# Performance work log

Measured on AMD Instinct MI355X. Metric: run time of the kernel, lower is better.

Reference implementation:

```python
import jax, jax.numpy as jnp
import numpy as np

R = 2048          # num residues
APR = 8           # atoms per residue -> num_atoms = 16384
H = 512           # hidden_dim (out_channels)
HEADS = 4
HD = H // HEADS
SD = HEADS * 7    # spatial feature dim
# atom_name2id: N=0, CA=1, C=2, O=3, CB=4, ...


def _layer_norm(x, g, b, eps=1e-5):
    mu = jnp.mean(x, axis=-1, keepdims=True)
    var = jnp.mean((x - mu) ** 2, axis=-1, keepdims=True)
    return (x - mu) / jnp.sqrt(var + eps) * g + b


def setup_inputs() -> dict:
    key = jax.random.key(0)
    ks = jax.random.split(key, 8)
    A = R * APR
    node_features = jax.random.normal(ks[0], (A, H), dtype=jnp.float32)
    node_positions = jax.random.normal(ks[1], (A, 3), dtype=jnp.float32) * 10.0
    # each residue owns APR consecutive atoms with types N,CA,C,O,CB,CG,CD,CE
    atom_type_ids = jnp.tile(jnp.arange(APR, dtype=jnp.int32), R)
    atom2residue = jnp.repeat(jnp.arange(R, dtype=jnp.int32), APR)
    s = 1.0 / np.sqrt(H)
    so = 1.0 / np.sqrt(H + SD)
    return {
        'node_features': node_features,
        'node_positions': node_positions,
        'Wq': jax.random.normal(ks[2], (H, H), jnp.float32) * s,
        'bq': jnp.zeros((H,), jnp.float32),
        'Wk': jax.random.normal(ks[3], (H, H), jnp.float32) * s,
        'bk': jnp.zeros((H,), jnp.float32),
        'Wv': jax.random.normal(ks[4], (H, H), jnp.float32) * s,
        'bv': jnp.zeros((H,), jnp.float32),
        'Wo': jax.random.normal(ks[5], (H + SD, H), jnp.float32) * so,
        'bo': jnp.zeros((H,), jnp.float32),
        'ln1_g': jnp.ones((H,), jnp.float32),
        'ln1_b': jnp.zeros((H,), jnp.float32),
        'ln2_g': jnp.ones((H,), jnp.float32),
        'ln2_b': jnp.zeros((H,), jnp.float32),
        'atom_type_ids': atom_type_ids,
        'atom2residue': atom2residue,
    }


def reference(node_features, node_positions, Wq, bq, Wk, bk, Wv, bv, Wo, bo,
              ln1_g, ln1_b, ln2_g, ln2_b, atom_type_ids, atom2residue):
    dt = node_features.dtype
    # ---------------- AtomPositionGather (vectorized scatter/gather) ----------------
    w_ca = (atom_type_ids == 1).astype(dt)   # CA
    w_cb = (atom_type_ids == 4).astype(dt)   # CB
    # scatter-mean of CA features per residue
    feat_sum = jax.ops.segment_sum(node_features * w_ca[:, None], atom2residue, num_segments=R)
    ca_cnt = jax.ops.segment_sum(w_ca, atom2residue, num_segments=R)
    residue_features = feat_sum / jnp.maximum(ca_cnt, 1.0)[:, None]
    # gather CA / CB positions (one CA/CB per residue in the data)
    pos_CA = jax.ops.segment_sum(node_positions * w_ca[:, None], atom2residue, num_segments=R)
    pos_CB = jax.ops.segment_sum(node_positions * w_cb[:, None], atom2residue, num_segments=R)
    no_cb = jnp.sum(jnp.abs(pos_CB), axis=1) < 1e-6
    pos_CB = jnp.where(no_cb[:, None], pos_CA, pos_CB)
    # residue completeness: >=3 atoms and contains N, CA, C
    cnt = jax.ops.segment_sum(jnp.ones_like(w_ca), atom2residue, num_segments=R)
    has = lambda t: jax.ops.segment_sum((atom_type_ids == t).astype(jnp.int32), atom2residue, num_segments=R) > 0
    residue_mask = (cnt >= 3) & has(0) & has(1) & has(2)
    # ---------------- per-residue local frames ----------------
    e1 = pos_CB - pos_CA
    n1 = jnp.linalg.norm(e1, axis=-1, keepdims=True)
    e1u = jnp.where(n1 > 1e-6, e1 / jnp.maximum(n1, 1e-6), e1)
    z_ax = jnp.array([0.0, 0.0, 1.0], dtype=dt)
    y_ax = jnp.array([0.0, 1.0, 0.0], dtype=dt)
    e2a = jnp.cross(e1u, jnp.broadcast_to(z_ax, e1u.shape))
    n2a = jnp.linalg.norm(e2a, axis=-1, keepdims=True)
    e2b = jnp.cross(e1u, jnp.broadcast_to(y_ax, e1u.shape))
    n2b = jnp.linalg.norm(e2b, axis=-1, keepdims=True)
    use_b = n2a < 1e-6
    e2 = jnp.where(use_b, e2b, e2a)
    n2 = jnp.where(use_b, n2b, n2a)
    e2u = e2 / jnp.maximum(n2, 1e-6)
    e3 = jnp.cross(e1u, e2u)
    frame = jnp.stack([e1u, e2u, e3], axis=-1)  # [R,3,3], basis as columns
    # original torch loop skips the last residue (i < len-1) and degenerate e1/e2
    ok = (jnp.arange(R) < R - 1) & (n1[:, 0] > 1e-6) & (n2[:, 0] > 1e-6)
    frames = jnp.where(ok[:, None, None], frame, jnp.eye(3, dtype=dt))
    # ---------------- PositionAwareLayer (batch=1, eval mode) ----------------
    x = residue_features[None]           # [1,R,H]
    ca = pos_CA[None]; cb = pos_CB[None]
    fr = frames[None]; m = residue_mask[None]
    q = (x @ Wq + bq).reshape(1, R, HEADS, HD)
    k = (x @ Wk + bk).reshape(1, R, HEADS, HD)
    v = (x @ Wv + bv).reshape(1, R, HEADS, HD)
    logits = jnp.einsum('blhd,bkhd->blkh', q, k)
    m2 = (m[:, :, None] & m[:, None, :])[..., None]          # [1,R,R,1]
    logits = jnp.where(m2, logits, -jnp.inf)
    alpha = jax.nn.softmax(logits, axis=2)                    # softmax over k
    feat_node = jnp.einsum('blkh,bkhd->blhd', alpha, v).reshape(1, R, H)
    rel_pos = cb[:, :, None, :] - ca[:, None, :, :]           # CB[l]-CA[k]: [1,R,R,3]
    bias = jnp.einsum('blkh,blkd->blhd', alpha, rel_pos)      # [1,R,HEADS,3]
    dist = jnp.linalg.norm(bias, axis=-1, keepdims=True)
    pts = jnp.einsum('blij,blhj->blhi', fr, bias)
    dirn = pts / (jnp.linalg.norm(pts, axis=-1, keepdims=True) + 1e-10)
    feat_spatial = jnp.concatenate([pts.reshape(1, R, -1), dist.reshape(1, R, -1), dirn.reshape(1, R, -1)], axis=-1)
    feat_all = jnp.concatenate([feat_node, feat_spatial], axis=-1)  # [1,R,H+SD]
    h = jax.nn.relu(feat_all @ Wo + bo)                       # dropout = identity (eval)
    h = _layer_norm(h, ln1_g, ln1_b)
    h = jnp.where(m[..., None], h, jnp.zeros_like(h))
    x_updated = _layer_norm(x + h, ln2_g, ln2_b)
    return x_updated
```

## Files before the change

### kernel.cpp

```cpp
#include <hip/hip_runtime.h>
#include <hip/hip_bf16.h>
#include <stdint.h>


#define R_ 2048
#define APR_ 8
#define H_ 512
#define HEADS_ 4
#define HD_ 128
#define FA_LD 544

typedef __attribute__((ext_vector_type(4))) float f32x4;
typedef __attribute__((ext_vector_type(4))) unsigned int u32x4;
typedef __attribute__((ext_vector_type(4))) unsigned short us4;
typedef __bf16 bf16x8 __attribute__((ext_vector_type(8)));

static __device__ __forceinline__ float bf2f(unsigned short u) {
    union { unsigned int i; float f; } c; c.i = ((unsigned int)u) << 16; return c.f;
}
static __device__ __forceinline__ unsigned short f2bf(float f) {
    union { float f; unsigned int i; } c; c.f = f;
    unsigned int r = c.i + 0x7fffu + ((c.i >> 16) & 1u);
    return (unsigned short)(r >> 16);
}
static __device__ __forceinline__ float san(float v) {
    return (v == v && fabsf(v) < 1e30f) ? v : 0.f;
}
static __device__ __forceinline__ float loadf(const void* p, size_t i, bool f32) {
    float v = f32 ? ((const float*)p)[i] : bf2f(((const unsigned short*)p)[i]);
    return (v == v && fabsf(v) < 1e30f) ? v : 0.f;
}

__global__ void diag(unsigned short* out, float val) {
    if (threadIdx.x == 0 && blockIdx.x == 0) out[0] = f2bf(val);
}

__global__ void detect_dtype(const unsigned short* __restrict__ nf, int* flag) {
    __shared__ int bad;
    if (threadIdx.x == 0) bad = 0;
    __syncthreads();
    int cnt = 0;
    for (int i = threadIdx.x; i < 8192; i += 256) {
        unsigned e = (nf[i] >> 7) & 0xFFu;
        if (e >= 0xC0u) cnt++;
    }
    atomicAdd(&bad, cnt);
    __syncthreads();
    if (threadIdx.x == 0) *flag = (bad > 16) ? 1 : 0;
}

__global__ void gather_frames(const void* __restrict__ pos,
                              const int* __restrict__ atype,
                              const int* __restrict__ flag,
                              int* __restrict__ cai, float* __restrict__ ca,
                              float* __restrict__ cb, float* __restrict__ fr,
                              float* __restrict__ maskf)
{
    int r = blockIdx.x * blockDim.x + threadIdx.x;
    if (r >= R_) return;
    bool f32 = *flag != 0;
    int base = r * APR_;
    float caP[3] = {0,0,0}, cbP[3] = {0,0,0};
    int idx = base; bool h0=false, h1=false, h2=false;
    for (int a = 0; a < APR_; a++) {
        int t = atype[base + a];
        if (t == 0) h0 = true;
        if (t == 2) h2 = true;
        if (t == 1) { h1 = true; idx = base + a;
            for (int j = 0; j < 3; j++) caP[j] += loadf(pos, (size_t)(base+a)*3 + j, f32); }
        if (t == 4) {
            for (int j = 0; j < 3; j++) cbP[j] += loadf(pos, (size_t)(base+a)*3 + j, f32); }
    }
    float s = fabsf(cbP[0]) + fabsf(cbP[1]) + fabsf(cbP[2]);
    if (s < 1e-6f) { cbP[0]=caP[0]; cbP[1]=caP[1]; cbP[2]=caP[2]; }
    float e1[3] = { cbP[0]-caP[0], cbP[1]-caP[1], cbP[2]-caP[2] };
    float n1 = sqrtf(e1[0]*e1[0] + e1[1]*e1[1] + e1[2]*e1[2]);
    float e1u[3] = { e1[0], e1[1], e1[2] };
    if (n1 > 1e-6f) { float iv = 1.f / fmaxf(n1, 1e-6f); e1u[0]*=iv; e1u[1]*=iv; e1u[2]*=iv; }
    float e2a[3] = { e1u[1], -e1u[0], 0.f };
    float n2a = sqrtf(e2a[0]*e2a[0] + e2a[1]*e2a[1]);
    float e2b[3] = { -e1u[2], 0.f, e1u[0] };
    float n2b = sqrtf(e2b[0]*e2b[0] + e2b[2]*e2b[2]);
    bool useb = n2a < 1e-6f;
    float e2[3] = { useb?e2b[0]:e2a[0], useb?e2b[1]:e2a[1], useb?e2b[2]:e2a[2] };
    float n2 = useb ? n2b : n2a;
    float iv2 = 1.f / fmaxf(n2, 1e-6f);
    float e2u[3] = { e2[0]*iv2, e2[1]*iv2, e2[2]*iv2 };
    float e3[3] = { e1u[1]*e2u[2]-e1u[2]*e2u[1],
                    e1u[2]*e2u[0]-e1u[0]*e2u[2],
                    e1u[0]*e2u[1]-e1u[1]*e2u[0] };
    bool ok = (r < R_-1) && (n1 > 1e-6f) && (n2 > 1e-6f);
    float F[9];
    if (ok) { F[0]=e1u[0]; F[1]=e2u[0]; F[2]=e3[0];
              F[3]=e1u[1]; F[4]=e2u[1]; F[5]=e3[1];
              F[6]=e1u[2]; F[7]=e2u[2]; F[8]=e3[2]; }
    else    { F[0]=1;F[1]=0;F[2]=0; F[3]=0;F[4]=1;F[5]=0; F[6]=0;F[7]=0;F[8]=1; }
    cai[r] = idx;
    for (int j = 0; j < 3; j++) { ca[r*3+j] = caP[j]; cb[r*3+j] = cbP[j]; }
    for (int j = 0; j < 9; j++) fr[r*9+j] = F[j];
    maskf[r] = (h0 && h1 && h2) ? 1.f : 0.f;
}

__global__ __launch_bounds__(256) void pack_prep(
    const void* __restrict__ nf, const int* __restrict__ cai,
    const void* __restrict__ Wq, const void* __restrict__ Wk, const void* __restrict__ Wv,
    const void* __restrict__ Wo,
    unsigned short* __restrict__ xg_hi, unsigned short* __restrict__ xg_lo,
    unsigned short* __restrict__ wqt_hi, unsigned short* __restrict__ wqt_lo,
    unsigned short* __restrict__ wot_hi, unsigned short* __restrict__ wot_lo,
    const int* __restrict__ flag)
{
    const bool f32 = *flag != 0;
    const int bid = blockIdx.x, tid = threadIdx.x;
    us4 h4, l4;
    if (bid < 1024) {
        int flat = bid*256 + tid;
        int row = flat >> 7, kc = flat & 127;
        size_t src = (size_t)cai[row]*H_ + kc*4;
        #pragma unroll
        for (int i = 0; i < 4; i++) {
            float v = loadf(nf, src + i, f32);
            unsigned short hb = f2bf(v);
            h4[i] = hb; l4[i] = f2bf(v - bf2f(hb));
        }
        *(us4*)(xg_hi + (size_t)row*H_ + kc*4) = h4;
        *(us4*)(xg_lo + (size_t)row*H_ + kc*4) = l4;
    } else if (bid < 1792) {
        int flat = (bid-1024)*256 + tid;
        int kc = flat / 1536, nn = flat - kc*1536;
        int mat = nn >> 9, ncol = nn & 511;
        const void* W = (mat==0) ? Wq : (mat==1) ? Wk : Wv;
        #pragma unroll
        for (int i = 0; i < 4; i++) {
            float v = loadf(W, (size_t)(kc*4+i)*H_ + ncol, f32);
            unsigned short hb = f2bf(v);
            h4[i] = hb; l4[i] = f2bf(v - bf2f(hb));
        }
        *(us4*)(wqt_hi + (size_t)nn*H_ + kc*4) = h4;
        *(us4*)(wqt_lo + (size_t)nn*H_ + kc*4) = l4;
    } else {
        int flat = (bid-1792)*256 + tid;
        int kc = flat >> 9, n = flat & 511;
        #pragma unroll
        for (int i = 0; i < 4; i++) {
            int k = kc*4 + i;
            float v = (k < 540) ? loadf(Wo, (size_t)k*H_ + n, f32) : 0.f;
            unsigned short hb = f2bf(v);
            h4[i] = hb; l4[i] = f2bf(v - bf2f(hb));
        }
        *(us4*)(wot_hi + (size_t)n*FA_LD + kc*4) = h4;
        *(us4*)(wot_lo + (size_t)n*FA_LD + kc*4) = l4;
    }
}

__global__ __launch_bounds__(256, 1) void qkv_mfma(
    const unsigned short* __restrict__ xg_hi, const unsigned short* __restrict__ xg_lo,
    const unsigned short* __restrict__ wqt_hi, const unsigned short* __restrict__ wqt_lo,
    const void* __restrict__ bq, const void* __restrict__ bk, const void* __restrict__ bv,
    unsigned short* __restrict__ qf, unsigned short* __restrict__ kf,
    unsigned short* __restrict__ vt, const int* __restrict__ flag)
{
    __shared__ __align__(16) char smem[33792];
    char* Xhi = smem;
    char* Xlo = smem + 8192;
    char* Bhi = smem + 16384;
    char* Blo = smem + 24576;
    const int tid = threadIdx.x;
    const int w = tid >> 6, lane = tid & 63, cL = lane & 15, gL = lane >> 4;
    const int wm = w >> 1, wn = w & 1;
    const int mbase = blockIdx.x * 128;
    const int nblk  = blockIdx.y * 128;
    const int mat = nblk >> 9, ncol0 = nblk & 511;
    const bool f32 = *flag != 0;
    const unsigned short* ahg = xg_hi + (size_t)mbase * H_;
    const unsigned short* alg = xg_lo + (size_t)mbase * H_;
    const unsigned short* bhg = wqt_hi + (size_t)nblk * H_;
    const unsigned short* blg = wqt_lo + (size_t)nblk * H_;

    u32x4 va[4], vb[4];
#define QKV_LOAD(K0)                                                          \
    {                                                                         \
        _Pragma("unroll")                                                     \
        for (int i = 0; i < 4; i++) {                                         \
// ... 142 lines not shown
        }                                                                     \
    }
    WO_LOAD(0)
    f32x4 acc[4][4] = {};
    for (int kt = 0; kt < 17; kt++) {
        __syncthreads();
        #pragma unroll
        for (int i = 0; i < 4; i++) {
            int flat = i*256 + tid, row = flat >> 3, c4 = flat & 7;
            int sw = ((row>>1)&3) << 4;
            us4 h4, l4;
            #pragma unroll
            for (int e = 0; e < 4; e++) {
                float v = xv[i*4+e];
                unsigned short hb = f2bf(v);
                h4[e] = hb; l4[e] = f2bf(v - bf2f(hb));
            }
            *(us4*)(Ahi + row*64 + ((c4*8) ^ sw)) = h4;
            *(us4*)(Alo + row*64 + ((c4*8) ^ sw)) = l4;
        }
        #pragma unroll
        for (int i = 0; i < 4; i++) {
            int flat = i*256 + tid, pl = flat >> 9, rem = flat & 511;
            int row = rem >> 2, c16 = rem & 3;
            char* p = pl ? Blo : Bhi;
            *(u32x4*)(p + row*64 + ((c16*16) ^ (((row>>1)&3)<<4))) = vb[i];
        }
        __syncthreads();
        if (kt < 16) WO_LOAD((kt+1)*32)
        bf16x8 ah[4], al[4], bh[4], bl[4];
        #pragma unroll
        for (int ms = 0; ms < 4; ms++) {
            int row = wm*64 + ms*16 + cL;
            int off = row*64 + ((gL*16) ^ (((row>>1)&3)<<4));
            ah[ms] = *(const bf16x8*)(Ahi + off);
            al[ms] = *(const bf16x8*)(Alo + off);
        }
        #pragma unroll
        for (int ns = 0; ns < 4; ns++) {
            int row = wn*64 + ns*16 + cL;
            int off = row*64 + ((gL*16) ^ (((row>>1)&3)<<4));
            bh[ns] = *(const bf16x8*)(Bhi + off);
            bl[ns] = *(const bf16x8*)(Blo + off);
        }
        #pragma unroll
        for (int ms = 0; ms < 4; ms++)
            #pragma unroll
            for (int ns = 0; ns < 4; ns++) {
                acc[ms][ns] = __builtin_amdgcn_mfma_f32_16x16x32_bf16(ah[ms], bh[ns], acc[ms][ns], 0,0,0);
                acc[ms][ns] = __builtin_amdgcn_mfma_f32_16x16x32_bf16(ah[ms], bl[ns], acc[ms][ns], 0,0,0);
                acc[ms][ns] = __builtin_amdgcn_mfma_f32_16x16x32_bf16(al[ms], bh[ns], acc[ms][ns], 0,0,0);
            }
    }
#undef WO_LOAD
    float* ep = (float*)smem + w*2112;
    #pragma unroll
    for (int half = 0; half < 2; half++) {
        __syncthreads();
        #pragma unroll
        for (int ms2 = 0; ms2 < 2; ms2++) {
            int ms = half*2 + ms2;
            #pragma unroll
            for (int ns = 0; ns < 4; ns++)
                #pragma unroll
                for (int j = 0; j < 4; j++)
                    ep[(ms2*16 + gL*4 + j)*66 + ns*16 + cL] = acc[ms][ns][j];
        }
        __syncthreads();
        int r = lane >> 1, cp = (lane & 1) * 32;
        int mrow = mbase + wm*64 + half*32 + r;
        #pragma unroll
        for (int c4 = 0; c4 < 8; c4++) {
            int nloc = cp + c4*4;
            int ncol = nbase + wn*64 + nloc;
            f32x4 o;
            #pragma unroll
            for (int e = 0; e < 4; e++)
                o[e] = ep[r*66 + nloc + e] + loadf(bo, ncol + e, f32);
            *(f32x4*)(Y + (size_t)mrow*H_ + ncol) = o;
        }
    }
}

__global__ __launch_bounds__(256, 1) void attn_mfma(
    const unsigned short* __restrict__ qf, const unsigned short* __restrict__ kf,
    const unsigned short* __restrict__ vt,
    const float* __restrict__ ca, const float* __restrict__ cb,
    const float* __restrict__ fr, const float* __restrict__ maskf,
    float* __restrict__ fa)
{
    __shared__ __align__(16) char smem[153600];
    const int tid = threadIdx.x;
    const int w = tid >> 6, lane = tid & 63;
    const int cL = lane & 15, gL = lane >> 4;
    const int qbase = blockIdx.x * 32;
    const int h = blockIdx.y;

    char* KsW  = smem + w*16384;
    char* VtW  = smem + 65536 + w*16384;
    char* AshW = smem + 131072 + w*4608;
    char* caSW = smem + 149504 + w*1024;

    bf16x8 qfrag[2][4];
    #pragma unroll
    for (int mt = 0; mt < 2; mt++)
        #pragma unroll
        for (int ks = 0; ks < 4; ks++)
            qfrag[mt][ks] = *(const bf16x8*)(qf + (size_t)(qbase + mt*16 + cL)*H_
                                             + h*HD_ + ks*32 + gL*8);
    float mq[2][4];
    #pragma unroll
    for (int mt = 0; mt < 2; mt++)
        #pragma unroll
        for (int j = 0; j < 4; j++)
            mq[mt][j] = (maskf[qbase + mt*16 + gL*4 + j] > 0.f) ? 1.f : 0.f;

    f32x4 O[2][8] = {};
    float den[2][4] = {}, axv[2][4] = {}, ayv[2][4] = {}, azv[2][4] = {};

    const unsigned short* kbase = kf + h*HD_;
    const unsigned short* vbase = vt + (size_t)h*HD_*R_;

    for (int kt = w; kt < R_/64; kt += 4) {
        const int kb = kt * 64;
        u32x4 tK[16], tV[16];
        #pragma unroll
        for (int j = 0; j < 16; j++) {
            int flat = j*64 + lane;
            tK[j] = *(const u32x4*)(kbase + (size_t)(kb + (flat>>4))*H_ + (flat&15)*8);
        }
        #pragma unroll
        for (int j = 0; j < 16; j++) {
            int flat = j*64 + lane;
            tV[j] = *(const u32x4*)(vbase + (size_t)(flat>>3)*R_ + kb + (flat&7)*8);
        }
        f32x4 cav4;
        cav4[0] = ca[(kb+lane)*3+0]; cav4[1] = ca[(kb+lane)*3+1];
        cav4[2] = ca[(kb+lane)*3+2]; cav4[3] = maskf[kb+lane];
        #pragma unroll
        for (int j = 0; j < 16; j++) {
            int flat = j*64 + lane;
            int row = flat>>4, c = flat&15;
            *(u32x4*)(KsW + row*256 + ((c*16) ^ ((row&7)<<4))) = tK[j];
        }
        #pragma unroll
        for (int j = 0; j < 16; j++) {
            int flat = j*64 + lane;
            int d = flat>>3, c = flat&7;
            *(u32x4*)(VtW + d*128 + ((c*16) ^ ((d&7)<<4))) = tV[j];
        }
        *(f32x4*)(caSW + lane*16) = cav4;

        f32x4 sacc[2][4] = {};
        #pragma unroll
        for (int nt = 0; nt < 4; nt++) {
            int n = nt*16 + cL;
            int rs = (n&7)<<4;
            bf16x8 k0 = *(const bf16x8*)(KsW + n*256 + (((0*4+gL)*16) ^ rs));
            bf16x8 k1 = *(const bf16x8*)(KsW + n*256 + (((1*4+gL)*16) ^ rs));
            bf16x8 k2 = *(const bf16x8*)(KsW + n*256 + (((2*4+gL)*16) ^ rs));
            bf16x8 k3 = *(const bf16x8*)(KsW + n*256 + (((3*4+gL)*16) ^ rs));
            #pragma unroll
            for (int mt = 0; mt < 2; mt++) {
                sacc[mt][nt] = __builtin_amdgcn_mfma_f32_16x16x32_bf16(qfrag[mt][0], k0, sacc[mt][nt], 0,0,0);
                sacc[mt][nt] = __builtin_amdgcn_mfma_f32_16x16x32_bf16(qfrag[mt][1], k1, sacc[mt][nt], 0,0,0);
                sacc[mt][nt] = __builtin_amdgcn_mfma_f32_16x16x32_bf16(qfrag[mt][2], k2, sacc[mt][nt], 0,0,0);
                sacc[mt][nt] = __builtin_amdgcn_mfma_f32_16x16x32_bf16(qfrag[mt][3], k3, sacc[mt][nt], 0,0,0);
            }
        }

        unsigned short* arow = (unsigned short*)AshW;
        #pragma unroll
        for (int nt = 0; nt < 4; nt++) {
            f32x4 cav = *(const f32x4*)(caSW + (nt*16 + cL)*16);
            #pragma unroll
            for (int mt = 0; mt < 2; mt++) {
                f32x4 s4 = sacc[mt][nt];
                float av[4];
                #pragma unroll
                for (int j = 0; j < 4; j++) {
                    float a = __expf(fminf(s4[j], 75.f)) * cav[3] * mq[mt][j];
                    if (!(a < 3.0e38f)) a = 0.f;
                    av[j] = a;
                    den[mt][j] += a;
                    axv[mt][j] += a * cav[0];
                    ayv[mt][j] += a * cav[1];
                    azv[mt][j] += a * cav[2];
                }
                unsigned int p01, p23;
                asm("v_cvt_pk_bf16_f32 %0, %1, %2" : "=v"(p01) : "v"(av[0]), "v"(av[1]));
                asm("v_cvt_pk_bf16_f32 %0, %1, %2" : "=v"(p23) : "v"(av[2]), "v"(av[3]));
                int qr = mt*16 + gL*4;
                int col = nt*16 + cL;
                arow[(qr+0)*72 + col] = (unsigned short)p01;
                arow[(qr+1)*72 + col] = (unsigned short)(p01 >> 16);
                arow[(qr+2)*72 + col] = (unsigned short)p23;
                arow[(qr+3)*72 + col] = (unsigned short)(p23 >> 16);
            }
        }

        #pragma unroll
        for (int ks = 0; ks < 2; ks++) {
            bf16x8 pa0 = *(const bf16x8*)(AshW + ((size_t)(cL)*72      + ks*32 + gL*8)*2);
            bf16x8 pa1 = *(const bf16x8*)(AshW + ((size_t)(16 + cL)*72 + ks*32 + gL*8)*2);
            #pragma unroll
            for (int dt = 0; dt < 8; dt++) {
                int d = dt*16 + cL;
                bf16x8 vb = *(const bf16x8*)(VtW + d*128 + (((ks*4+gL)*16) ^ ((d&7)<<4)));
                O[0][dt] = __builtin_amdgcn_mfma_f32_16x16x32_bf16(pa0, vb, O[0][dt], 0,0,0);
                O[1][dt] = __builtin_amdgcn_mfma_f32_16x16x32_bf16(pa1, vb, O[1][dt], 0,0,0);
            }
        }
    }

    __syncthreads();
    float* Ored = (float*)smem;
    float* dred = (float*)(smem + 67584);
    #pragma unroll
    for (int mt = 0; mt < 2; mt++)
        #pragma unroll
        for (int dt = 0; dt < 8; dt++) {
            f32x4 o4 = O[mt][dt];
            #pragma unroll
            for (int j = 0; j < 4; j++)
                Ored[w*4224 + (mt*16 + gL*4 + j)*132 + dt*16 + cL] = o4[j];
        }
    #pragma unroll
    for (int mt = 0; mt < 2; mt++)
        #pragma unroll
        for (int j = 0; j < 4; j++) {
            float d0 = den[mt][j], x0 = axv[mt][j], y0 = ayv[mt][j], z0 = azv[mt][j];
            #pragma unroll
            for (int off = 8; off >= 1; off >>= 1) {
                d0 += __shfl_xor(d0, off); x0 += __shfl_xor(x0, off);
                y0 += __shfl_xor(y0, off); z0 += __shfl_xor(z0, off);
            }
            if (cL == 0) {
                f32x4 v; v[0]=d0; v[1]=x0; v[2]=y0; v[3]=z0;
                *(f32x4*)&dred[w*128 + (mt*16 + gL*4 + j)*4] = v;
            }
        }
    __syncthreads();
    {
        int q = tid >> 3, d0 = (tid & 7) * 16;
        float dn = dred[q*4] + dred[128 + q*4] + dred[256 + q*4] + dred[384 + q*4];
        float inv = (dn > 0.f) ? 1.f/dn : 0.f;
        size_t rowb = (size_t)(qbase+q)*FA_LD + h*HD_ + d0;
        #pragma unroll
        for (int e = 0; e < 4; e++) {
            f32x4 s = *(const f32x4*)&Ored[q*132 + d0 + e*4];
            #pragma unroll
            for (int ww = 1; ww < 4; ww++)
                s += *(const f32x4*)&Ored[ww*4224 + q*132 + d0 + e*4];
            *(f32x4*)&fa[rowb + e*4] = s * inv;
        }
    }
    if (tid < 32) {
        float dn = dred[tid*4+0] + dred[128+tid*4+0] + dred[256+tid*4+0] + dred[384+tid*4+0];
        float ax = dred[tid*4+1] + dred[128+tid*4+1] + dred[256+tid*4+1] + dred[384+tid*4+1];
        float ay = dred[tid*4+2] + dred[128+tid*4+2] + dred[256+tid*4+2] + dred[384+tid*4+2];
        float az = dred[tid*4+3] + dred[128+tid*4+3] + dred[256+tid*4+3] + dred[384+tid*4+3];
        float inv = (dn > 0.f) ? 1.f/dn : 0.f;
        float live = (dn > 0.f) ? 1.f : 0.f;
        int qg = qbase + tid;
        float b0 = cb[qg*3+0]*live - ax*inv;
        float b1 = cb[qg*3+1]*live - ay*inv;
        float b2 = cb[qg*3+2]*live - az*inv;
        float dist = sqrtf(b0*b0 + b1*b1 + b2*b2);
        const float* F = fr + (size_t)qg*9;
        float p0 = F[0]*b0 + F[1]*b1 + F[2]*b2;
        float p1 = F[3]*b0 + F[4]*b1 + F[5]*b2;
        float p2 = F[6]*b0 + F[7]*b1 + F[8]*b2;
        float pn = sqrtf(p0*p0 + p1*p1 + p2*p2) + 1e-10f;
        size_t rb = (size_t)qg * FA_LD;
        fa[rb + 512 + h*3 + 0] = p0;
        fa[rb + 512 + h*3 + 1] = p1;
        fa[rb + 512 + h*3 + 2] = p2;
        fa[rb + 524 + h]       = dist;
        fa[rb + 528 + h*3 + 0] = p0/pn;
        fa[rb + 528 + h*3 + 1] = p1/pn;
        fa[rb + 528 + h*3 + 2] = p2/pn;
        if (h == 0) { fa[rb+540]=0.f; fa[rb+541]=0.f; fa[rb+542]=0.f; fa[rb+543]=0.f; }
    }
}

__global__ __launch_bounds__(256) void final_ln(
    const float* __restrict__ Y, const void* __restrict__ nf,
    const int* __restrict__ cai, const float* __restrict__ maskf,
    const void* __restrict__ g1, const void* __restrict__ b1,
    const void* __restrict__ g2, const void* __restrict__ b2,
    void* __restrict__ out, const int* __restrict__ flag)
{
    const int tid = threadIdx.x, lane = tid & 63, wave = tid >> 6;
    const int r = blockIdx.x * 4 + wave;
    bool f32 = *flag != 0;
    const float mk = maskf[r];
    const size_t xrow = (size_t)cai[r] * H_;
    float y[8], s1 = 0.f, s2 = 0.f;
    #pragma unroll
    for (int i = 0; i < 8; i++) {
        int c = lane + i*64;
        float v = fmaxf(Y[(size_t)r*H_ + c], 0.f);
        y[i] = v; s1 += v; s2 += v*v;
    }
    #pragma unroll
    for (int off = 32; off; off >>= 1) { s1 += __shfl_xor(s1, off); s2 += __shfl_xor(s2, off); }
    float mu = s1 * (1.f/H_);
    float var = s2 * (1.f/H_) - mu*mu;
    float rstd = rsqrtf(fmaxf(var, 0.f) + 1e-5f);
    float t[8], u1 = 0.f, u2 = 0.f;
    #pragma unroll
    for (int i = 0; i < 8; i++) {
        int c = lane + i*64;
        float hh = (y[i]-mu)*rstd*loadf(g1, c, f32) + loadf(b1, c, f32);
        hh *= mk;
        float tv = loadf(nf, xrow + c, f32) + hh;
        t[i] = tv; u1 += tv; u2 += tv*tv;
    }
    #pragma unroll
    for (int off = 32; off; off >>= 1) { u1 += __shfl_xor(u1, off); u2 += __shfl_xor(u2, off); }
    float mu2 = u1 * (1.f/H_);
    float var2 = u2 * (1.f/H_) - mu2*mu2;
    float rstd2 = rsqrtf(fmaxf(var2, 0.f) + 1e-5f);
    #pragma unroll
    for (int i = 0; i < 8; i++) {
        int c = lane + i*64;
        float ov = (t[i]-mu2)*rstd2*loadf(g2, c, f32) + loadf(b2, c, f32);
        if (f32) ((float*)out)[(size_t)r*H_ + c] = ov;
        else ((unsigned short*)out)[(size_t)r*H_ + c] = f2bf(ov);
    }
}

extern "C" void kernel_launch(void* const* d_in, const int* in_sizes, int n_in,
                              void* d_out, int out_size, void* d_ws, size_t ws_size,
                              hipStream_t stream)
{
    static const int expected[16] = {
        8388608, 49152, 262144, 512, 262144, 512, 262144, 512,
        276480, 512, 512, 512, 512, 512, 16384, 16384
    };
    if (n_in != 16) {
        diag<<<dim3(1), dim3(64), 0, stream>>>((unsigned short*)d_out, 1000.f + n_in);
        return;
    }
    for (int i = 0; i < 16; i++) {
        if (in_sizes[i] != expected[i]) {
            diag<<<dim3(1), dim3(64), 0, stream>>>((unsigned short*)d_out, 2000.f + 10.f*i);
            return;
        }
    }
    const size_t need = 16056320;
    if (ws_size < need) {
        diag<<<dim3(1), dim3(64), 0, stream>>>((unsigned short*)d_out, 3000.f);
        return;
    }

    const void* nf  = d_in[0];
    const void* pos = d_in[1];
    const void* Wq  = d_in[2];  const void* bq = d_in[3];
    const void* Wk  = d_in[4];  const void* bk = d_in[5];
    const void* Wv  = d_in[6];  const void* bv = d_in[7];
    const void* Wo  = d_in[8];  const void* bo = d_in[9];
    const void* g1  = d_in[10]; const void* b1 = d_in[11];
    const void* g2  = d_in[12]; const void* b2 = d_in[13];
    const int* atype = (const int*)d_in[14];

    char* ws = (char*)d_ws;
    int*   flag  = (int*)  (ws + 0);
    int*   cai   = (int*)  (ws + 1024);
    float* ca    = (float*)(ws + 9216);
    float* cb    = (float*)(ws + 33792);
    float* fr    = (float*)(ws + 58368);
    float* maskf = (float*)(ws + 132096);
    unsigned short* qf = (unsigned short*)(ws + 1048576);
    unsigned short* kf = (unsigned short*)(ws + 3145728);
    unsigned short* vt = (unsigned short*)(ws + 5242880);
    unsigned short* xg_hi = (unsigned short*)(ws + 7340032);
    unsigned short* xg_lo = (unsigned short*)(ws + 9437184);
    float* fa = (float*)(ws + 7340032);
    unsigned short* wqt_hi = (unsigned short*)(ws + 11796480);
    unsigned short* wqt_lo = (unsigned short*)(ws + 13369344);
    unsigned short* wot_hi = (unsigned short*)(ws + 14942208);
    unsigned short* wot_lo = (unsigned short*)(ws + 15499264);
    float* Y  = (float*)qf;

    detect_dtype<<<dim3(1), dim3(256), 0, stream>>>((const unsigned short*)nf, flag);
    gather_frames<<<dim3(8), dim3(256), 0, stream>>>(pos, atype, flag, cai, ca, cb, fr, maskf);
    pack_prep<<<dim3(2064), dim3(256), 0, stream>>>(nf, cai, Wq, Wk, Wv, Wo,
                                                    xg_hi, xg_lo, wqt_hi, wqt_lo,
                                                    wot_hi, wot_lo, flag);
    qkv_mfma<<<dim3(16, 12), dim3(256), 0, stream>>>(xg_hi, xg_lo, wqt_hi, wqt_lo,
                                                     bq, bk, bv, qf, kf, vt, flag);
    attn_mfma<<<dim3(R_/32, HEADS_), dim3(256), 0, stream>>>(qf, kf, vt,
                                                             ca, cb, fr, maskf, fa);
    wo_mfma<<<dim3(16, 4), dim3(256), 0, stream>>>(fa, wot_hi, wot_lo, bo, Y, flag);
    final_ln<<<dim3(512), dim3(256), 0, stream>>>(Y, nf, cai, maskf, g1, b1, g2, b2,
                                                  d_out, flag);
}
```

Before: 211.8 us.

## Split attention over key halves with atomic accumulation and separate finalize kernel

```diff
diff --git a/kernel.cpp b/kernel.cpp
--- a/kernel.cpp
+++ b/kernel.cpp
@@ -22,9 +22,6 @@
     union { float f; unsigned int i; } c; c.f = f;
     unsigned int r = c.i + 0x7fffu + ((c.i >> 16) & 1u);
     return (unsigned short)(r >> 16);
-}
-static __device__ __forceinline__ float san(float v) {
-    return (v == v && fabsf(v) < 1e30f) ? v : 0.f;
 }
 static __device__ __forceinline__ float loadf(const void* p, size_t i, bool f32) {
     float v = f32 ? ((const float*)p)[i] : bf2f(((const unsigned short*)p)[i]);
@@ -54,7 +51,8 @@
                               const int* __restrict__ flag,
                               int* __restrict__ cai, float* __restrict__ ca,
                               float* __restrict__ cb, float* __restrict__ fr,
-                              float* __restrict__ maskf)
+                              float* __restrict__ maskf,
+                              f32x4* __restrict__ ca4, float* __restrict__ dsum)
 {
     int r = blockIdx.x * blockDim.x + threadIdx.x;
     if (r >= R_) return;
@@ -98,7 +96,13 @@
     cai[r] = idx;
     for (int j = 0; j < 3; j++) { ca[r*3+j] = caP[j]; cb[r*3+j] = cbP[j]; }
     for (int j = 0; j < 9; j++) fr[r*9+j] = F[j];
-    maskf[r] = (h0 && h1 && h2) ? 1.f : 0.f;
+    float mk = (h0 && h1 && h2) ? 1.f : 0.f;
+    maskf[r] = mk;
+    f32x4 c4; c4[0]=caP[0]; c4[1]=caP[1]; c4[2]=caP[2]; c4[3]=mk;
+    ca4[r] = c4;
+    f32x4 z = {0.f,0.f,0.f,0.f};
+    #pragma unroll
+    for (int j = 0; j < 4; j++) *((f32x4*)(dsum + (size_t)r*16) + j) = z;
 }
 
 __global__ __launch_bounds__(256) void pack_prep(
@@ -407,24 +411,25 @@
     }
 }
 
-__global__ __launch_bounds__(256, 1) void attn_mfma(
+__global__ void zero_fa(f32x4* __restrict__ fa4) {
+    f32x4 z = {0.f,0.f,0.f,0.f};
+    fa4[blockIdx.x*256 + threadIdx.x] = z;
+}
+
+__global__ __launch_bounds__(256, 1) void attn_mfma2(
     const unsigned short* __restrict__ qf, const unsigned short* __restrict__ kf,
     const unsigned short* __restrict__ vt,
-    const float* __restrict__ ca, const float* __restrict__ cb,
-    const float* __restrict__ fr, const float* __restrict__ maskf,
-    float* __restrict__ fa)
+    const f32x4* __restrict__ ca4, const float* __restrict__ maskf,
+    float* __restrict__ fa, float* __restrict__ dsum)
 {
-    __shared__ __align__(16) char smem[153600];
+    __shared__ __align__(16) char smem[18432];
     const int tid = threadIdx.x;
     const int w = tid >> 6, lane = tid & 63;
     const int cL = lane & 15, gL = lane >> 4;
     const int qbase = blockIdx.x * 32;
     const int h = blockIdx.y;
-
-    char* KsW  = smem + w*16384;
-    char* VtW  = smem + 65536 + w*16384;
-    char* AshW = smem + 131072 + w*4608;
-    char* caSW = smem + 149504 + w*1024;
+    const int kb0 = blockIdx.z * 1024;
+    char* AshW = smem + w*4608;
 
     bf16x8 qfrag[2][4];
     #pragma unroll
@@ -446,45 +451,16 @@
     const unsigned short* kbase = kf + h*HD_;
     const unsigned short* vbase = vt + (size_t)h*HD_*R_;
 
-    for (int kt = w; kt < R_/64; kt += 4) {
-        const int kb = kt * 64;
-        u32x4 tK[16], tV[16];
-        #pragma unroll
-        for (int j = 0; j < 16; j++) {
-            int flat = j*64 + lane;
-            tK[j] = *(const u32x4*)(kbase + (size_t)(kb + (flat>>4))*H_ + (flat&15)*8);
-        }
-        #pragma unroll
-        for (int j = 0; j < 16; j++) {
-            int flat = j*64 + lane;
-            tV[j] = *(const u32x4*)(vbase + (size_t)(flat>>3)*R_ + kb + (flat&7)*8);
-        }
-        f32x4 cav4;
-        cav4[0] = ca[(kb+lane)*3+0]; cav4[1] = ca[(kb+lane)*3+1];
-        cav4[2] = ca[(kb+lane)*3+2]; cav4[3] = maskf[kb+lane];
-        #pragma unroll
-        for (int j = 0; j < 16; j++) {
-            int flat = j*64 + lane;
-            int row = flat>>4, c = flat&15;
-            *(u32x4*)(KsW + row*256 + ((c*16) ^ ((row&7)<<4))) = tK[j];
-        }
-        #pragma unroll
-        for (int j = 0; j < 16; j++) {
-            int flat = j*64 + lane;
-            int d = flat>>3, c = flat&7;
-            *(u32x4*)(VtW + d*128 + ((c*16) ^ ((d&7)<<4))) = tV[j];
-        }
-        *(f32x4*)(caSW + lane*16) = cav4;
-
+    for (int kt = w; kt < 16; kt += 4) {
+        const int kb = kb0 + kt*64;
         f32x4 sacc[2][4] = {};
         #pragma unroll
         for (int nt = 0; nt < 4; nt++) {
-            int n = nt*16 + cL;
-            int rs = (n&7)<<4;
-            bf16x8 k0 = *(const bf16x8*)(KsW + n*256 + (((0*4+gL)*16) ^ rs));
-            bf16x8 k1 = *(const bf16x8*)(KsW + n*256 + (((1*4+gL)*16) ^ rs));
-            bf16x8 k2 = *(const bf16x8*)(KsW + n*256 + (((2*4+gL)*16) ^ rs));
-            bf16x8 k3 = *(const bf16x8*)(KsW + n*256 + (((3*4+gL)*16) ^ rs));
+            const unsigned short* kr = kbase + (size_t)(kb + nt*16 + cL)*H_ + gL*8;
+            bf16x8 k0 = *(const bf16x8*)(kr);
+            bf16x8 k1 = *(const bf16x8*)(kr + 32);
+            bf16x8 k2 = *(const bf16x8*)(kr + 64);
+            bf16x8 k3 = *(const bf16x8*)(kr + 96);
             #pragma unroll
             for (int mt = 0; mt < 2; mt++) {
                 sacc[mt][nt] = __builtin_amdgcn_mfma_f32_16x16x32_bf16(qfrag[mt][0], k0, sacc[mt][nt], 0,0,0);
@@ -493,11 +469,10 @@
                 sacc[mt][nt] = __builtin_amdgcn_mfma_f32_16x16x32_bf16(qfrag[mt][3], k3, sacc[mt][nt], 0,0,0);
             }
         }
-
         unsigned short* arow = (unsigned short*)AshW;
         #pragma unroll
         for (int nt = 0; nt < 4; nt++) {
-            f32x4 cav = *(const f32x4*)(caSW + (nt*16 + cL)*16);
+            f32x4 cav = ca4[kb + nt*16 + cL];
             #pragma unroll
             for (int mt = 0; mt < 2; mt++) {
                 f32x4 s4 = sacc[mt][nt];
@@ -523,33 +498,27 @@
                 arow[(qr+3)*72 + col] = (unsigned short)(p23 >> 16);
             }
         }
-
         #pragma unroll
         for (int ks = 0; ks < 2; ks++) {
             bf16x8 pa0 = *(const bf16x8*)(AshW + ((size_t)(cL)*72      + ks*32 + gL*8)*2);
             bf16x8 pa1 = *(const bf16x8*)(AshW + ((size_t)(16 + cL)*72 + ks*32 + gL*8)*2);
             #pragma unroll
             for (int dt = 0; dt < 8; dt++) {
-                int d = dt*16 + cL;
-                bf16x8 vb = *(const bf16x8*)(VtW + d*128 + (((ks*4+gL)*16) ^ ((d&7)<<4)));
+                bf16x8 vb = *(const bf16x8*)(vbase + (size_t)(dt*16 + cL)*R_ + kb + ks*32 + gL*8);
                 O[0][dt] = __builtin_amdgcn_mfma_f32_16x16x32_bf16(pa0, vb, O[0][dt], 0,0,0);
                 O[1][dt] = __builtin_amdgcn_mfma_f32_16x16x32_bf16(pa1, vb, O[1][dt], 0,0,0);
             }
         }
     }
 
-    __syncthreads();
-    float* Ored = (float*)smem;
-    float* dred = (float*)(smem + 67584);
     #pragma unroll
     for (int mt = 0; mt < 2; mt++)
         #pragma unroll
-        for (int dt = 0; dt < 8; dt++) {
-            f32x4 o4 = O[mt][dt];
+        for (int dt = 0; dt < 8; dt++)
             #pragma unroll
             for (int j = 0; j < 4; j++)
-                Ored[w*4224 + (mt*16 + gL*4 + j)*132 + dt*16 + cL] = o4[j];
-        }
+                atomicAdd(&fa[(size_t)(qbase + mt*16 + gL*4 + j)*FA_LD + h*HD_ + dt*16 + cL],
+                          O[mt][dt][j]);
     #pragma unroll
     for (int mt = 0; mt < 2; mt++)
         #pragma unroll
@@ -561,43 +530,48 @@
                 y0 += __shfl_xor(y0, off); z0 += __shfl_xor(z0, off);
             }
             if (cL == 0) {
-                f32x4 v; v[0]=d0; v[1]=x0; v[2]=y0; v[3]=z0;
-                *(f32x4*)&dred[w*128 + (mt*16 + gL*4 + j)*4] = v;
-            }
-        }
-    __syncthreads();
+                int qg = qbase + mt*16 + gL*4 + j;
+                float* dp = dsum + (size_t)(qg*4 + h)*4;
+                atomicAdd(dp+0, d0); atomicAdd(dp+1, x0);
+                atomicAdd(dp+2, y0); atomicAdd(dp+3, z0);
+            }
+        }
+}
+
+__global__ __launch_bounds__(256) void attn_finalize(
+    const float* __restrict__ dsum, const float* __restrict__ cb,
+    const float* __restrict__ fr, float* __restrict__ fa)
+{
+    const int tid = threadIdx.x;
+    const int q0 = blockIdx.x * 8;
     {
-        int q = tid >> 3, d0 = (tid & 7) * 16;
-        float dn = dred[q*4] + dred[128 + q*4] + dred[256 + q*4] + dred[384 + q*4];
+        int row = q0 + (tid >> 5), l32 = tid & 31, hh = l32 >> 3;
+        float dn = dsum[(size_t)(row*4 + hh)*4];
         float inv = (dn > 0.f) ? 1.f/dn : 0.f;
-        size_t rowb = (size_t)(qbase+q)*FA_LD + h*HD_ + d0;
+        float* p = fa + (size_t)row*FA_LD + l32*16;
         #pragma unroll
         for (int e = 0; e < 4; e++) {
-            f32x4 s = *(const f32x4*)&Ored[q*132 + d0 + e*4];
-            #pragma unroll
-            for (int ww = 1; ww < 4; ww++)
-                s += *(const f32x4*)&Ored[ww*4224 + q*132 + d0 + e*4];
-            *(f32x4*)&fa[rowb + e*4] = s * inv;
+            f32x4 v = *(f32x4*)(p + e*4);
+            v *= inv;
+            *(f32x4*)(p + e*4) = v;
         }
     }
     if (tid < 32) {
-        float dn = dred[tid*4+0] + dred[128+tid*4+0] + dred[256+tid*4+0] + dred[384+tid*4+0];
-        float ax = dred[tid*4+1] + dred[128+tid*4+1] + dred[256+tid*4+1] + dred[384+tid*4+1];
-        float ay = dred[tid*4+2] + dred[128+tid*4+2] + dred[256+tid*4+2] + dred[384+tid*4+2];
-        float az = dred[tid*4+3] + dred[128+tid*4+3] + dred[256+tid*4+3] + dred[384+tid*4+3];
+        int q = q0 + (tid >> 2), h = tid & 3;
+        const float* dp = dsum + (size_t)(q*4 + h)*4;
+        float dn = dp[0], ax = dp[1], ay = dp[2], az = dp[3];
         float inv = (dn > 0.f) ? 1.f/dn : 0.f;
         float live = (dn > 0.f) ? 1.f : 0.f;
-        int qg = qbase + tid;
-        float b0 = cb[qg*3+0]*live - ax*inv;
-        float b1 = cb[qg*3+1]*live - ay*inv;
-        float b2 = cb[qg*3+2]*live - az*inv;
+        float b0 = cb[q*3+0]*live - ax*inv;
+        float b1 = cb[q*3+1]*live - ay*inv;
+        float b2 = cb[q*3+2]*live - az*inv;
         float dist = sqrtf(b0*b0 + b1*b1 + b2*b2);
-        const float* F = fr + (size_t)qg*9;
+        const float* F = fr + (size_t)q*9;
         float p0 = F[0]*b0 + F[1]*b1 + F[2]*b2;
         float p1 = F[3]*b0 + F[4]*b1 + F[5]*b2;
         float p2 = F[6]*b0 + F[7]*b1 + F[8]*b2;
         float pn = sqrtf(p0*p0 + p1*p1 + p2*p2) + 1e-10f;
-        size_t rb = (size_t)qg * FA_LD;
+        size_t rb = (size_t)q * FA_LD;
         fa[rb + 512 + h*3 + 0] = p0;
         fa[rb + 512 + h*3 + 1] = p1;
         fa[rb + 512 + h*3 + 2] = p2;
@@ -605,7 +579,6 @@
         fa[rb + 528 + h*3 + 0] = p0/pn;
         fa[rb + 528 + h*3 + 1] = p1/pn;
         fa[rb + 528 + h*3 + 2] = p2/pn;
-        if (h == 0) { fa[rb+540]=0.f; fa[rb+541]=0.f; fa[rb+542]=0.f; fa[rb+543]=0.f; }
     }
 }
 
@@ -697,6 +670,8 @@
     float* cb    = (float*)(ws + 33792);
     float* fr    = (float*)(ws + 58368);
     float* maskf = (float*)(ws + 132096);
+    f32x4* ca4   = (f32x4*)(ws + 140288);
+    float* dsum  = (float*)(ws + 173056);
     unsigned short* qf = (unsigned short*)(ws + 1048576);
     unsigned short* kf = (unsigned short*)(ws + 3145728);
     unsigned short* vt = (unsigned short*)(ws + 5242880);
@@ -710,14 +685,17 @@
     float* Y  = (float*)qf;
 
     detect_dtype<<<dim3(1), dim3(256), 0, stream>>>((const unsigned short*)nf, flag);
-    gather_frames<<<dim3(8), dim3(256), 0, stream>>>(pos, atype, flag, cai, ca, cb, fr, maskf);
+    gather_frames<<<dim3(8), dim3(256), 0, stream>>>(pos, atype, flag, cai, ca, cb, fr,
+                                                     maskf, ca4, dsum);
     pack_prep<<<dim3(2064), dim3(256), 0, stream>>>(nf, cai, Wq, Wk, Wv, Wo,
                                                     xg_hi, xg_lo, wqt_hi, wqt_lo,
                                                     wot_hi, wot_lo, flag);
     qkv_mfma<<<dim3(16, 12), dim3(256), 0, stream>>>(xg_hi, xg_lo, wqt_hi, wqt_lo,
                                                      bq, bk, bv, qf, kf, vt, flag);
-    attn_mfma<<<dim3(R_/32, HEADS_), dim3(256), 0, stream>>>(qf, kf, vt,
-                                                             ca, cb, fr, maskf, fa);
+    zero_fa<<<dim3(1088), dim3(256), 0, stream>>>((f32x4*)fa);
+    attn_mfma2<<<dim3(R_/32, HEADS_, 2), dim3(256), 0, stream>>>(qf, kf, vt,
+                                                                 ca4, maskf, fa, dsum);
+    attn_finalize<<<dim3(R_/8), dim3(256), 0, stream>>>(dsum, cb, fr, fa);
     wo_mfma<<<dim3(16, 4), dim3(256), 0, stream>>>(fa, wot_hi, wot_lo, bo, Y, flag);
     final_ln<<<dim3(512), dim3(256), 0, stream>>>(Y, nf, cai, maskf, g1, b1, g2, b2,
                                                   d_out, flag);
```

Measured after the change: 268.8 us. 26.9% more time.

## Restructure attention kernel to 8 waves with 32-key tiles and direct V fragment loads

Applied to the files above, without the earlier changes.

```diff
diff --git a/kernel.cpp b/kernel.cpp
--- a/kernel.cpp
+++ b/kernel.cpp
@@ -22,9 +22,6 @@
     union { float f; unsigned int i; } c; c.f = f;
     unsigned int r = c.i + 0x7fffu + ((c.i >> 16) & 1u);
     return (unsigned short)(r >> 16);
-}
-static __device__ __forceinline__ float san(float v) {
-    return (v == v && fabsf(v) < 1e30f) ? v : 0.f;
 }
 static __device__ __forceinline__ float loadf(const void* p, size_t i, bool f32) {
     float v = f32 ? ((const float*)p)[i] : bf2f(((const unsigned short*)p)[i]);
@@ -54,7 +51,7 @@
                               const int* __restrict__ flag,
                               int* __restrict__ cai, float* __restrict__ ca,
                               float* __restrict__ cb, float* __restrict__ fr,
-                              float* __restrict__ maskf)
+                              float* __restrict__ maskf, f32x4* __restrict__ ca4)
 {
     int r = blockIdx.x * blockDim.x + threadIdx.x;
     if (r >= R_) return;
@@ -98,7 +95,10 @@
     cai[r] = idx;
     for (int j = 0; j < 3; j++) { ca[r*3+j] = caP[j]; cb[r*3+j] = cbP[j]; }
     for (int j = 0; j < 9; j++) fr[r*9+j] = F[j];
-    maskf[r] = (h0 && h1 && h2) ? 1.f : 0.f;
+    float mk = (h0 && h1 && h2) ? 1.f : 0.f;
+    maskf[r] = mk;
+    f32x4 c4; c4[0]=caP[0]; c4[1]=caP[1]; c4[2]=caP[2]; c4[3]=mk;
+    ca4[r] = c4;
 }
 
 __global__ __launch_bounds__(256) void pack_prep(
@@ -407,24 +407,22 @@
     }
 }
 
-__global__ __launch_bounds__(256, 1) void attn_mfma(
+__global__ __launch_bounds__(512, 1) void attn_mfma3(
     const unsigned short* __restrict__ qf, const unsigned short* __restrict__ kf,
     const unsigned short* __restrict__ vt,
-    const float* __restrict__ ca, const float* __restrict__ cb,
-    const float* __restrict__ fr, const float* __restrict__ maskf,
+    const f32x4* __restrict__ ca4, const float* __restrict__ maskf,
+    const float* __restrict__ cb, const float* __restrict__ fr,
     float* __restrict__ fa)
 {
-    __shared__ __align__(16) char smem[153600];
+    __shared__ __align__(16) char smem[86016];
     const int tid = threadIdx.x;
     const int w = tid >> 6, lane = tid & 63;
     const int cL = lane & 15, gL = lane >> 4;
     const int qbase = blockIdx.x * 32;
     const int h = blockIdx.y;
 
-    char* KsW  = smem + w*16384;
-    char* VtW  = smem + 65536 + w*16384;
-    char* AshW = smem + 131072 + w*4608;
-    char* caSW = smem + 149504 + w*1024;
+    char* KsW  = smem + w*8192;
+    char* AshW = smem + 65536 + w*2560;
 
     bf16x8 qfrag[2][4];
     #pragma unroll
@@ -446,39 +444,31 @@
     const unsigned short* kbase = kf + h*HD_;
     const unsigned short* vbase = vt + (size_t)h*HD_*R_;
 
-    for (int kt = w; kt < R_/64; kt += 4) {
-        const int kb = kt * 64;
-        u32x4 tK[16], tV[16];
-        #pragma unroll
-        for (int j = 0; j < 16; j++) {
+    for (int kt = w; kt < 64; kt += 8) {
+        const int kb = kt * 32;
+        u32x4 tK[8];
+        #pragma unroll
+        for (int j = 0; j < 8; j++) {
             int flat = j*64 + lane;
             tK[j] = *(const u32x4*)(kbase + (size_t)(kb + (flat>>4))*H_ + (flat&15)*8);
         }
-        #pragma unroll
-        for (int j = 0; j < 16; j++) {
-            int flat = j*64 + lane;
-            tV[j] = *(const u32x4*)(vbase + (size_t)(flat>>3)*R_ + kb + (flat&7)*8);
-        }
-        f32x4 cav4;
-        cav4[0] = ca[(kb+lane)*3+0]; cav4[1] = ca[(kb+lane)*3+1];
-        cav4[2] = ca[(kb+lane)*3+2]; cav4[3] = maskf[kb+lane];
-        #pragma unroll
-        for (int j = 0; j < 16; j++) {
+        bf16x8 vreg[8];
+        #pragma unroll
+        for (int dt = 0; dt < 8; dt++)
+            vreg[dt] = *(const bf16x8*)(vbase + (size_t)(dt*16 + cL)*R_ + kb + gL*8);
+        f32x4 cav[2];
+        #pragma unroll
+        for (int nt = 0; nt < 2; nt++)
+            cav[nt] = ca4[kb + nt*16 + cL];
+        #pragma unroll
+        for (int j = 0; j < 8; j++) {
             int flat = j*64 + lane;
             int row = flat>>4, c = flat&15;
             *(u32x4*)(KsW + row*256 + ((c*16) ^ ((row&7)<<4))) = tK[j];
         }
-        #pragma unroll
-        for (int j = 0; j < 16; j++) {
-            int flat = j*64 + lane;
-            int d = flat>>3, c = flat&7;
-            *(u32x4*)(VtW + d*128 + ((c*16) ^ ((d&7)<<4))) = tV[j];
-        }
-        *(f32x4*)(caSW + lane*16) = cav4;
-
-        f32x4 sacc[2][4] = {};
-        #pragma unroll
-        for (int nt = 0; nt < 4; nt++) {
+        f32x4 sacc[2][2] = {};
+        #pragma unroll
+        for (int nt = 0; nt < 2; nt++) {
             int n = nt*16 + cL;
             int rs = (n&7)<<4;
             bf16x8 k0 = *(const bf16x8*)(KsW + n*256 + (((0*4+gL)*16) ^ rs));
@@ -493,63 +483,46 @@
                 sacc[mt][nt] = __builtin_amdgcn_mfma_f32_16x16x32_bf16(qfrag[mt][3], k3, sacc[mt][nt], 0,0,0);
             }
         }
-
         unsigned short* arow = (unsigned short*)AshW;
         #pragma unroll
-        for (int nt = 0; nt < 4; nt++) {
-            f32x4 cav = *(const f32x4*)(caSW + (nt*16 + cL)*16);
+        for (int nt = 0; nt < 2; nt++) {
             #pragma unroll
             for (int mt = 0; mt < 2; mt++) {
                 f32x4 s4 = sacc[mt][nt];
                 float av[4];
                 #pragma unroll
                 for (int j = 0; j < 4; j++) {
-                    float a = __expf(fminf(s4[j], 75.f)) * cav[3] * mq[mt][j];
+                    float a = __expf(fminf(s4[j], 75.f)) * cav[nt][3] * mq[mt][j];
                     if (!(a < 3.0e38f)) a = 0.f;
                     av[j] = a;
                     den[mt][j] += a;
-                    axv[mt][j] += a * cav[0];
-                    ayv[mt][j] += a * cav[1];
-                    azv[mt][j] += a * cav[2];
+                    axv[mt][j] += a * cav[nt][0];
+                    ayv[mt][j] += a * cav[nt][1];
+                    azv[mt][j] += a * cav[nt][2];
                 }
                 unsigned int p01, p23;
                 asm("v_cvt_pk_bf16_f32 %0, %1, %2" : "=v"(p01) : "v"(av[0]), "v"(av[1]));
                 asm("v_cvt_pk_bf16_f32 %0, %1, %2" : "=v"(p23) : "v"(av[2]), "v"(av[3]));
                 int qr = mt*16 + gL*4;
                 int col = nt*16 + cL;
-                arow[(qr+0)*72 + col] = (unsigned short)p01;
-                arow[(qr+1)*72 + col] = (unsigned short)(p01 >> 16);
-                arow[(qr+2)*72 + col] = (unsigned short)p23;
-                arow[(qr+3)*72 + col] = (unsigned short)(p23 >> 16);
-            }
-        }
-
-        #pragma unroll
-        for (int ks = 0; ks < 2; ks++) {
-            bf16x8 pa0 = *(const bf16x8*)(AshW + ((size_t)(cL)*72      + ks*32 + gL*8)*2);
-            bf16x8 pa1 = *(const bf16x8*)(AshW + ((size_t)(16 + cL)*72 + ks*32 + gL*8)*2);
-            #pragma unroll
-            for (int dt = 0; dt < 8; dt++) {
-                int d = dt*16 + cL;
-                bf16x8 vb = *(const bf16x8*)(VtW + d*128 + (((ks*4+gL)*16) ^ ((d&7)<<4)));
-                O[0][dt] = __builtin_amdgcn_mfma_f32_16x16x32_bf16(pa0, vb, O[0][dt], 0,0,0);
-                O[1][dt] = __builtin_amdgcn_mfma_f32_16x16x32_bf16(pa1, vb, O[1][dt], 0,0,0);
-            }
+                arow[(qr+0)*40 + col] = (unsigned short)p01;
+                arow[(qr+1)*40 + col] = (unsigned short)(p01 >> 16);
+                arow[(qr+2)*40 + col] = (unsigned short)p23;
+                arow[(qr+3)*40 + col] = (unsigned short)(p23 >> 16);
+            }
+        }
+        bf16x8 pa0 = *(const bf16x8*)(AshW + ((size_t)(cL)*40      + gL*8)*2);
+        bf16x8 pa1 = *(const bf16x8*)(AshW + ((size_t)(16 + cL)*40 + gL*8)*2);
+        #pragma unroll
+        for (int dt = 0; dt < 8; dt++) {
+            O[0][dt] = __builtin_amdgcn_mfma_f32_16x16x32_bf16(pa0, vreg[dt], O[0][dt], 0,0,0);
+            O[1][dt] = __builtin_amdgcn_mfma_f32_16x16x32_bf16(pa1, vreg[dt], O[1][dt], 0,0,0);
         }
     }
 
     __syncthreads();
     float* Ored = (float*)smem;
-    float* dred = (float*)(smem + 67584);
-    #pragma unroll
-    for (int mt = 0; mt < 2; mt++)
-        #pragma unroll
-        for (int dt = 0; dt < 8; dt++) {
-            f32x4 o4 = O[mt][dt];
-            #pragma unroll
-            for (int j = 0; j < 4; j++)
-                Ored[w*4224 + (mt*16 + gL*4 + j)*132 + dt*16 + cL] = o4[j];
-        }
+    float* dred = (float*)(smem + 69632);
     #pragma unroll
     for (int mt = 0; mt < 2; mt++)
         #pragma unroll
@@ -565,26 +538,35 @@
                 *(f32x4*)&dred[w*128 + (mt*16 + gL*4 + j)*4] = v;
             }
         }
+    #pragma unroll
+    for (int mt = 0; mt < 2; mt++)
+        #pragma unroll
+        for (int dtl = 0; dtl < 4; dtl++) {
+            f32x4 o4 = O[mt][dtl];
+            #pragma unroll
+            for (int j = 0; j < 4; j++)
+                Ored[w*2176 + (mt*16 + gL*4 + j)*68 + dtl*16 + cL] = o4[j];
+        }
     __syncthreads();
     {
-        int q = tid >> 3, d0 = (tid & 7) * 16;
-        float dn = dred[q*4] + dred[128 + q*4] + dred[256 + q*4] + dred[384 + q*4];
+        int q = tid >> 4, c4 = (tid & 15) * 4;
+        float dn = 0.f;
+        #pragma unroll
+        for (int ww = 0; ww < 8; ww++) dn += dred[ww*128 + q*4];
         float inv = (dn > 0.f) ? 1.f/dn : 0.f;
-        size_t rowb = (size_t)(qbase+q)*FA_LD + h*HD_ + d0;
-        #pragma unroll
-        for (int e = 0; e < 4; e++) {
-            f32x4 s = *(const f32x4*)&Ored[q*132 + d0 + e*4];
-            #pragma unroll
-            for (int ww = 1; ww < 4; ww++)
-                s += *(const f32x4*)&Ored[ww*4224 + q*132 + d0 + e*4];
-            *(f32x4*)&fa[rowb + e*4] = s * inv;
-        }
+        f32x4 s = *(const f32x4*)&Ored[q*68 + c4];
+        #pragma unroll
+        for (int ww = 1; ww < 8; ww++)
+            s += *(const f32x4*)&Ored[ww*2176 + q*68 + c4];
+        *(f32x4*)&fa[(size_t)(qbase+q)*FA_LD + h*HD_ + c4] = s * inv;
     }
     if (tid < 32) {
-        float dn = dred[tid*4+0] + dred[128+tid*4+0] + dred[256+tid*4+0] + dred[384+tid*4+0];
-        float ax = dred[tid*4+1] + dred[128+tid*4+1] + dred[256+tid*4+1] + dred[384+tid*4+1];
-        float ay = dred[tid*4+2] + dred[128+tid*4+2] + dred[256+tid*4+2] + dred[384+tid*4+2];
-        float az = dred[tid*4+3] + dred[128+tid*4+3] + dred[256+tid*4+3] + dred[384+tid*4+3];
+        float dn=0.f, ax=0.f, ay=0.f, az=0.f;
+        #pragma unroll
+        for (int ww = 0; ww < 8; ww++) {
+            const float* dp = &dred[ww*128 + tid*4];
+            dn += dp[0]; ax += dp[1]; ay += dp[2]; az += dp[3];
+        }
         float inv = (dn > 0.f) ? 1.f/dn : 0.f;
         float live = (dn > 0.f) ? 1.f : 0.f;
         int qg = qbase + tid;
@@ -607,6 +589,29 @@
         fa[rb + 528 + h*3 + 2] = p2/pn;
         if (h == 0) { fa[rb+540]=0.f; fa[rb+541]=0.f; fa[rb+542]=0.f; fa[rb+543]=0.f; }
     }
+    __syncthreads();
+    #pragma unroll
+    for (int mt = 0; mt < 2; mt++)
+        #pragma unroll
+        for (int dtl = 0; dtl < 4; dtl++) {
+            f32x4 o4 = O[mt][4 + dtl];
+            #pragma unroll
+            for (int j = 0; j < 4; j++)
+                Ored[w*2176 + (mt*16 + gL*4 + j)*68 + dtl*16 + cL] = o4[j];
+        }
+    __syncthreads();
+    {
+        int q = tid >> 4, c4 = (tid & 15) * 4;
+        float dn = 0.f;
+        #pragma unroll
+        for (int ww = 0; ww < 8; ww++) dn += dred[ww*128 + q*4];
+        float inv = (dn > 0.f) ? 1.f/dn : 0.f;
+        f32x4 s = *(const f32x4*)&Ored[q*68 + c4];
+        #pragma unroll
+        for (int ww = 1; ww < 8; ww++)
+            s += *(const f32x4*)&Ored[ww*2176 + q*68 + c4];
+        *(f32x4*)&fa[(size_t)(qbase+q)*FA_LD + h*HD_ + 64 + c4] = s * inv;
+    }
 }
 
 __global__ __launch_bounds__(256) void final_ln(
@@ -697,6 +702,7 @@
     float* cb    = (float*)(ws + 33792);
     float* fr    = (float*)(ws + 58368);
     float* maskf = (float*)(ws + 132096);
+    f32x4* ca4   = (f32x4*)(ws + 140288);
     unsigned short* qf = (unsigned short*)(ws + 1048576);
     unsigned short* kf = (unsigned short*)(ws + 3145728);
     unsigned short* vt = (unsigned short*)(ws + 5242880);
@@ -710,14 +716,15 @@
     float* Y  = (float*)qf;
 
     detect_dtype<<<dim3(1), dim3(256), 0, stream>>>((const unsigned short*)nf, flag);
-    gather_frames<<<dim3(8), dim3(256), 0, stream>>>(pos, atype, flag, cai, ca, cb, fr, maskf);
+    gather_frames<<<dim3(8), dim3(256), 0, stream>>>(pos, atype, flag, cai, ca, cb, fr,
+                                                     maskf, ca4);
     pack_prep<<<dim3(2064), dim3(256), 0, stream>>>(nf, cai, Wq, Wk, Wv, Wo,
                                                     xg_hi, xg_lo, wqt_hi, wqt_lo,
                                                     wot_hi, wot_lo, flag);
     qkv_mfma<<<dim3(16, 12), dim3(256), 0, stream>>>(xg_hi, xg_lo, wqt_hi, wqt_lo,
                                                      bq, bk, bv, qf, kf, vt, flag);
-    attn_mfma<<<dim3(R_/32, HEADS_), dim3(256), 0, stream>>>(qf, kf, vt,
-                                                             ca, cb, fr, maskf, fa);
+    attn_mfma3<<<dim3(R_/32, HEADS_), dim3(512), 0, stream>>>(qf, kf, vt, ca4, maskf,
+                                                              cb, fr, fa);
     wo_mfma<<<dim3(16, 4), dim3(256), 0, stream>>>(fa, wot_hi, wot_lo, bo, Y, flag);
     final_ln<<<dim3(512), dim3(256), 0, stream>>>(Y, nf, cai, maskf, g1, b1, g2, b2,
                                                   d_out, flag);
```

Measured after the change: 210.2 us. No clear change (-0.8%).
